# Optimization experiments

Measured on AMD Instinct MI355X. Metric: run time of the kernel, lower is better.

## Reference

```python
import jax, jax.numpy as jnp
import numpy as np

T, B, E, H, V = 128, 64, 300, 2048, 50000


def setup_inputs() -> dict:
    key = jax.random.key(0)
    ks = jax.random.split(key, 7)
    tokens = jax.random.randint(ks[0], (T, B), 0, V, dtype=jnp.int32)
    lens = jax.random.randint(ks[1], (B,), 1, T + 1, dtype=jnp.int32)  # lens >= 1 (assert 0 not in lens)
    embed_table = jax.random.normal(ks[2], (V, E), dtype=jnp.float32) * 0.1
    W_ih = jax.random.normal(ks[3], (4 * H, E), dtype=jnp.float32) * 0.02
    W_hh = jax.random.normal(ks[4], (4 * H, H), dtype=jnp.float32) * 0.02
    b_ih = jax.random.normal(ks[5], (4 * H,), dtype=jnp.float32) * 0.02
    b_hh = jax.random.normal(ks[6], (4 * H,), dtype=jnp.float32) * 0.02
    return {"tokens": tokens, "lens": lens, "embed_table": embed_table,
            "W_ih": W_ih, "W_hh": W_hh, "b_ih": b_ih, "b_hh": b_hh}


def _lstm_scan(xs, W_ih, W_hh, bias, reverse):
    # xs: [T, B, E]; returns all hidden states [T, B, H] (in scan order) and final (h, c)
    hdim = W_hh.shape[1]
    bsz = xs.shape[1]
    h0 = jnp.zeros((bsz, hdim), xs.dtype)
    c0 = jnp.zeros((bsz, hdim), xs.dtype)

    def step(carry, x):
        h, c = carry
        gates = x @ W_ih.T + h @ W_hh.T + bias  # [B, 4H]
        i, f, g, o = jnp.split(gates, 4, axis=-1)  # PyTorch LSTMCell gate order: i, f, g, o
        i = jax.nn.sigmoid(i)
        f = jax.nn.sigmoid(f)
        g = jnp.tanh(g)
        o = jax.nn.sigmoid(o)
        c = f * c + i * g
        h = o * jnp.tanh(c)
        return (h, c), h

    (h_fin, c_fin), hs = jax.lax.scan(step, (h0, c0), xs, reverse=reverse)
    return hs, h_fin


def reference(tokens, lens, embed_table, W_ih, W_hh, b_ih, b_hh):
    # tokens: [T, B] int ids (time-major, matching input_[i] loop over dim 0)
    x = embed_table[tokens]  # [T, B, E]
    bias = b_ih + b_hh
    hs_fwd, _ = _lstm_scan(x, W_ih, W_hh, bias, reverse=False)   # [T, B, H]
    _, h_bwd = _lstm_scan(x, W_ih, W_hh, bias, reverse=True)     # [B, H], same shared cell
    bsz = tokens.shape[1]
    # forward hidden at the last valid timestep of each example (lens - 1)
    last_fwd = hs_fwd[lens - 1, jnp.arange(bsz)]  # [B, H]
    return jnp.concatenate([last_fwd, h_bwd], axis=1)  # [B, 2H]
```

## Files before the change

kernel.cpp:

```cpp
#include <hip/hip_runtime.h>
#include <math.h>

#define T_ 128
#define B_ 64
#define E_ 300
#define H_ 2048

#define K1   2368
#define XKS  10
#define NKS  74
#define APELEMS 19398656ull
#define BXELEMS 5242880ull
#define BHPING  524288ull

typedef __attribute__((ext_vector_type(8))) short short8;
typedef __attribute__((ext_vector_type(4))) float float4v;

__device__ __forceinline__ unsigned f2bf(float f) {
    unsigned u = __float_as_uint(f);
    return (u + 0x7FFFu + ((u >> 16) & 1u)) >> 16;
}
__device__ __forceinline__ float bf2f(unsigned b) { return __uint_as_float(b << 16); }

__device__ __forceinline__ void gl_lds16(const void* g, void* l) {
    __builtin_amdgcn_global_load_lds(
        (const __attribute__((address_space(1))) unsigned int*)g,
        (__attribute__((address_space(3))) unsigned int*)l, 16, 0, 0);
}

__device__ __forceinline__ float sigm(float x) { return 1.f / (1.f + expf(-x)); }


__global__ void init2(short* __restrict__ Bh, float* __restrict__ cb) {
    const int nB = 2 * (int)BHPING;
    const int nC = 2 * 2048 * 64;
    int stride = gridDim.x * blockDim.x;
    int i = blockIdx.x * blockDim.x + threadIdx.x;
    for (int idx = i; idx < nB; idx += stride) Bh[idx] = 0;
    for (int idx = i; idx < nC; idx += stride) cb[idx] = 0.f;
}

__global__ void pack_w(const float* __restrict__ Wih, const float* __restrict__ Whh,
                       short* __restrict__ Ahi, short* __restrict__ Alo) {
    long long idx = (long long)blockIdx.x * blockDim.x + threadIdx.x;
    if (idx >= (long long)APELEMS) return;
    int j  = (int)(idx & 7);
    int l  = (int)((idx >> 3) & 63);
    int mf = (int)((idx >> 9) & 7);
    int rest = (int)(idx >> 12);
    int ks = rest % 74;
    int rb = rest / 74;
    int row = rb * 128 + mf * 16 + (l & 15);
    int kr  = ks * 32 + (l >> 4) * 8 + j;
    float wv = 0.f;
    if (kr < 300)       wv = Wih[(size_t)row * 300 + kr];
    else if (kr >= 320) wv = Whh[(size_t)row * 2048 + (kr - 320)];
    unsigned hb = f2bf(wv);
    Ahi[idx] = (short)hb;
    Alo[idx] = (short)f2bf(wv - bf2f(hb));
}

__global__ void pack_x(const int* __restrict__ tokens, const float* __restrict__ embed,
                       short* __restrict__ Bx) {
    long long idx = (long long)blockIdx.x * blockDim.x + threadIdx.x;
    if (idx >= (long long)BXELEMS) return;
    int j   = (int)(idx & 7);
    int l   = (int)((idx >> 3) & 63);
    int nf4 = (int)((idx >> 9) & 3);
    int hl  = (int)((idx >> 11) & 1);
    int rest = (int)(idx >> 12);
    int ks = rest % 10;
    int tt = rest / 10;
    int b  = nf4 * 16 + (l & 15);
    int kr = ks * 32 + (l >> 4) * 8 + j;
    float v = 0.f;
    if (kr < 300) {
        int tok = tokens[tt * 64 + b];
        v = embed[(size_t)tok * 300 + kr];
    }
    unsigned hb = f2bf(v);
    Bx[idx] = hl ? (short)f2bf(v - bf2f(hb)) : (short)hb;
}

template<int BLD>
__device__ __forceinline__ void stage_tile(
    const short* __restrict__ Ap, const short* __restrict__ Bx,
    const short* __restrict__ Bh, short* lds,
    int mb, int ks, int buf, int t, int ping, int tid)
{
    short* As = lds + buf * 12288;
    short* Bs = As + 4096;
#pragma unroll
    for (int q = 0; q < 2; ++q) {
        int lid = q * 256 + tid;
        gl_lds16(Ap + (size_t)(mb * 74 + ks) * 4096 + lid * 8, As + lid * 8);
    }
#pragma unroll
    for (int q = 0; q < BLD; ++q) {
        int lid = q * 256 + tid;
        int g = lid >> 6, ll = lid & 63;
        int dsel, hl, nf4;
        if (BLD == 2) { dsel = g >> 2; hl = 0;            nf4 = g & 3; }
        else          { dsel = g >> 3; hl = (g >> 2) & 1; nf4 = g & 3; }
        const short* src;
        if (ks < XKS) {
            int xt = dsel ? (127 - t) : t;
            src = Bx + (((size_t)(xt * 10 + ks) * 2 + hl) * 4 + nf4) * 512 + ll * 8;
        } else {
            src = Bh + (size_t)ping * BHPING
                + ((size_t)(ks - 10) * 16 + (dsel * 2 + hl) * 4 + nf4) * 512 + ll * 8;
        }
        gl_lds16(src, Bs + lid * 8);
    }
}

__global__ __launch_bounds__(256, 2) void gemm_step(
    const short* __restrict__ Ahi, const short* __restrict__ Alo,
    const short* __restrict__ Bx, const short* __restrict__ Bh,
    float* __restrict__ p, int t)
{
    __shared__ short lds[36864];
    const int bb = (int)blockIdx.x;
    const int mb = bb >> 3, s = bb & 7;
    const int tid = (int)threadIdx.x;
    const int w = tid >> 6, l = tid & 63;
    const int wm = w >> 1, wn = w & 1;
    const int ping = t & 1;
    const int ks0 = (s < 2) ? s * 10 : 20 + (s - 2) * 9;
    const int nks = (s < 2) ? 10 : 9;

    float4v acc[4][4];
#pragma unroll
    for (int i = 0; i < 4; ++i)
#pragma unroll
        for (int n = 0; n < 4; ++n) acc[i][n] = (float4v){0.f, 0.f, 0.f, 0.f};

    stage_tile<4>(Ahi, Bx, Bh, lds, mb, ks0,     0, t, ping, tid);
    stage_tile<4>(Ahi, Bx, Bh, lds, mb, ks0 + 1, 1, t, ping, tid);
    asm volatile("s_waitcnt vmcnt(6)" ::: "memory");
    __builtin_amdgcn_s_barrier();
    __builtin_amdgcn_sched_barrier(0);

    for (int it = 0; it < nks; ++it) {
        const int buf = it % 3;
        stage_tile<4>(Ahi, Bx, Bh, lds, mb, ks0 + it + 2, (it + 2) % 3, t, ping, tid);

        short* As = lds + buf * 12288;
        short* Bs = As + 4096;
        short8 a[4], bf[8];
#pragma unroll
        for (int i = 0; i < 4; ++i)
            a[i] = *(const short8*)(As + ((wm * 4 + i) * 64 + l) * 8);
#pragma unroll
        for (int j = 0; j < 8; ++j)
            bf[j] = *(const short8*)(Bs + ((wn * 8 + j) * 64 + l) * 8);
        __builtin_amdgcn_s_setprio(1);
#pragma unroll
        for (int i = 0; i < 4; ++i)
#pragma unroll
            for (int hl = 0; hl < 2; ++hl)
#pragma unroll
                for (int n = 0; n < 4; ++n)
                    acc[i][n] = __builtin_amdgcn_mfma_f32_16x16x32_bf16(
                        a[i], bf[hl * 4 + n], acc[i][n], 0, 0, 0);
        __builtin_amdgcn_s_setprio(0);

        asm volatile("s_waitcnt vmcnt(6)" ::: "memory");
        __builtin_amdgcn_s_barrier();
        __builtin_amdgcn_sched_barrier(0);
    }
    asm volatile("s_waitcnt vmcnt(0)" ::: "memory");
    __builtin_amdgcn_s_barrier();
    __builtin_amdgcn_sched_barrier(0);

    stage_tile<2>(Alo, Bx, Bh, lds, mb, ks0,     0, t, ping, tid);
    stage_tile<2>(Alo, Bx, Bh, lds, mb, ks0 + 1, 1, t, ping, tid);
    asm volatile("s_waitcnt vmcnt(4)" ::: "memory");
    __builtin_amdgcn_s_barrier();
    __builtin_amdgcn_sched_barrier(0);

    for (int it = 0; it < nks; ++it) {
        const int buf = it % 3;
        stage_tile<2>(Alo, Bx, Bh, lds, mb, ks0 + it + 2, (it + 2) % 3, t, ping, tid);

        short* As = lds + buf * 12288;
        short* Bs = As + 4096;
        short8 a[4], bf[4];
#pragma unroll
        for (int i = 0; i < 4; ++i)
            a[i] = *(const short8*)(As + ((wm * 4 + i) * 64 + l) * 8);
#pragma unroll
        for (int n = 0; n < 4; ++n)
            bf[n] = *(const short8*)(Bs + ((wn * 4 + n) * 64 + l) * 8);
        __builtin_amdgcn_s_setprio(1);
#pragma unroll
        for (int i = 0; i < 4; ++i)
#pragma unroll
            for (int n = 0; n < 4; ++n)
                acc[i][n] = __builtin_amdgcn_mfma_f32_16x16x32_bf16(
                    a[i], bf[n], acc[i][n], 0, 0, 0);
        __builtin_amdgcn_s_setprio(0);

        asm volatile("s_waitcnt vmcnt(4)" ::: "memory");
        __builtin_amdgcn_s_barrier();
        __builtin_amdgcn_sched_barrier(0);
    }
    asm volatile("s_waitcnt vmcnt(0)" ::: "memory");
    __builtin_amdgcn_s_barrier();
    __builtin_amdgcn_sched_barrier(0);

#pragma unroll
    for (int i = 0; i < 4; ++i)
#pragma unroll
        for (int n = 0; n < 4; ++n)
#pragma unroll
            for (int r = 0; r < 4; ++r) {
                int row = mb * 128 + wm * 64 + i * 16 + (l >> 4) * 4 + r;
                int col = wn * 64 + n * 16 + (l & 15);
                p[((size_t)s * 8192 + row) * 128 + col] = acc[i][n][r];
            }
}

__global__ __launch_bounds__(256) void update2(
    const float* __restrict__ p,
    const float* __restrict__ b_ih, const float* __restrict__ b_hh,
    const int* __restrict__ lens,
    float* __restrict__ cbuf,
    short* __restrict__ Bh,
    float* __restrict__ out, int t)
{
    int tid0 = blockIdx.x * 256 + threadIdx.x;
    for (int item = tid0; item < 262144; item += 65536) {
        int b = item & 63, k = (item >> 6) & 2047, dir = item >> 17;
        float g[4];
#pragma unroll
        for (int gg = 0; gg < 4; ++gg) {
            int row = gg * 2048 + k;
            float v = 0.f;
#pragma unroll
            for (int s = 0; s < 8; ++s) v += p[((size_t)s * 8192 + row) * 128 + dir * 64 + b];
            g[gg] = v + b_ih[row] + b_hh[row];
        }
        float iv = sigm(g[0]);
        float fv = sigm(g[1]);
        float gv = tanhf(g[2]);
        float ov = sigm(g[3]);
        size_t cidx = ((size_t)dir * 2048 + k) * 64 + b;
        float c = fv * cbuf[cidx] + iv * gv;
        cbuf[cidx] = c;
        float h = ov * tanhf(c);

        int kk = k & 31, ksh = k >> 5;
        int jj = kk & 7, ll = (kk >> 3) * 16 + (b & 15), sub = b >> 4;
        int pingW = (t + 1) & 1;
        size_t baseh = (size_t)pingW * BHPING + ((size_t)ksh * 16 + (dir * 2) * 4 + sub) * 512 + ll * 8 + jj;
        size_t basel = (size_t)pingW * BHPING + ((size_t)ksh * 16 + (dir * 2 + 1) * 4 + sub) * 512 + ll * 8 + jj;
        unsigned hb = f2bf(h);
        Bh[baseh] = (short)hb;
        Bh[basel] = (short)f2bf(h - bf2f(hb));

        if (dir == 0) { if (t == lens[b] - 1) out[(size_t)b * 4096 + k] = h; }
        else          { if (t == 127)         out[(size_t)b * 4096 + 2048 + k] = h; }
    }
}

#define R2K1    2368
#define R2EPAD  304
#define R2HOFF  304
#define R2HEND  2352
#define R2SEGSTEPS 74
#define R2REALSTEPS 222
#define R2SPLITSTEPS 56

__global__ void init_ws2(short* __restrict__ hb, float* __restrict__ cb,
                         short* __restrict__ zer) {
    const int nH = 2 * 2 * 2 * 64 * 2048;
    const int nC = 2 * 2048 * 64;
    int stride = gridDim.x * blockDim.x;
    int i = blockIdx.x * blockDim.x + threadIdx.x;
    for (int idx = i; idx < nH; idx += stride) hb[idx] = 0;
    for (int idx = i; idx < nC; idx += stride) cb[idx] = 0.f;
    for (int idx = i; idx < 128; idx += stride) zer[idx] = 0;
}

__global__ void conv_w(const float* __restrict__ Wih, const float* __restrict__ Whh,
                       short* __restrict__ whi, short* __restrict__ wlo) {
    int idx = blockIdx.x * blockDim.x + threadIdx.x;
    const int total = 8192 * R2K1;
    if (idx >= total) return;
    int j = idx / R2K1;
    int col = idx - j * R2K1;
    float w = 0.f;
    if (col < E_) w = Wih[(size_t)j * E_ + col];
    else if (col >= R2HOFF && col < R2HEND) w = Whh[(size_t)j * H_ + (col - R2HOFF)];
    unsigned hb = f2bf(w);
    whi[idx] = (short)hb;
    wlo[idx] = (short)f2bf(w - bf2f(hb));
}

__global__ void conv_x(const int* __restrict__ tokens, const float* __restrict__ embed,
                       short* __restrict__ xhi, short* __restrict__ xlo) {
    int idx = blockIdx.x * blockDim.x + threadIdx.x;
    const int total = T_ * B_ * R2EPAD;
    if (idx >= total) return;
    int t = idx / (B_ * R2EPAD);
    int r = idx - t * (B_ * R2EPAD);
    int bb = r / R2EPAD;
    int e = r - bb * R2EPAD;
    float v = 0.f;
    if (e < E_) {
        int tok = tokens[t * B_ + bb];
        v = embed[(size_t)tok * E_ + e];
    }
    unsigned hb = f2bf(v);
    xhi[idx] = (short)hb;
    xlo[idx] = (short)f2bf(v - bf2f(hb));
}

__global__ __launch_bounds__(512) void gemm_partial(
    const short* __restrict__ Whi, const short* __restrict__ Wlo,
    const short* __restrict__ xhi, const short* __restrict__ xlo,
    const short* __restrict__ hbuf,
    const short* __restrict__ zeros,
    float* __restrict__ pbuf, int t)
{
    __shared__ short As[2][8192];
    __shared__ short Bs[2][2048];

    const int bx  = blockIdx.x;
    const int s   = bx & 3;
    const int kt  = (bx >> 2) & 31;
    const int dir = bx >> 7;
    const int tid = threadIdx.x;
    const int w   = tid >> 6;
    const int l   = tid & 63;
    const int ping = t & 1;
    const int xt   = dir ? (T_ - 1 - t) : t;

    int jA[2], cA[2];
#pragma unroll
    for (int q = 0; q < 2; ++q) {
        int idx = (w * 2 + q) * 64 + l;
        cA[q] = idx >> 8;
        int row = idx & 255;
        jA[q] = (row >> 6) * 2048 + kt * 64 + (row & 63);
    }
    int cB = 0, bB = 0;
    if (w < 4) { int idx = w * 64 + l; cB = idx >> 6; bB = idx & 63; }

    const int lhi = l >> 4, llo = l & 15;
    const int rowbase = (w >> 1) * 64 + (w & 1) * 32;

    float4v acc[2][4];
#pragma unroll
    for (int a = 0; a < 2; ++a)
#pragma unroll
        for (int b = 0; b < 4; ++b) acc[a][b] = (float4v){0.f, 0.f, 0.f, 0.f};

    auto stage = [&](int g, int buf) {
        const bool dummy = (g >= R2REALSTEPS);
        const int seg = dummy ? 2 : g / R2SEGSTEPS;
        const int ss  = dummy ? 0 : g - seg * R2SEGSTEPS;
        const int kbase = ss * 32;
        const short* Wsel = (seg < 2) ? Whi : Wlo;
        const int hl = (seg == 1) ? 1 : 0;
        const short* xsel = (seg == 1) ? xlo : xhi;
        const short* hsel = hbuf + (((size_t)ping * 2 + hl) * 2 + dir) * (64 * 2048);
#pragma unroll
        for (int q = 0; q < 2; ++q) {
            const short* src = Wsel + (size_t)jA[q] * R2K1 + kbase + 8 * cA[q];
            gl_lds16(src, &As[buf][(w * 2 + q) * 64 * 8]);
        }
        if (w < 4) {
            int row8 = kbase + 8 * cB;
            const short* src;
            if (dummy || row8 >= R2HEND) src = zeros;
            else if (row8 < R2EPAD)      src = xsel + ((size_t)xt * 64 + bB) * R2EPAD + row8;
            else                         src = hsel + (size_t)bB * 2048 + (row8 - R2HOFF);
            gl_lds16(src, &Bs[buf][w * 64 * 8]);
        }
    };

    const int g0 = s * R2SPLITSTEPS;
    stage(g0, 0);

    for (int it = 0; it < R2SPLITSTEPS; ++it) {
        const int buf = it & 1;
        if (it + 1 < R2SPLITSTEPS) stage(g0 + it + 1, buf ^ 1);
        __syncthreads();
        short8 a0 = *(const short8*)&As[buf][(lhi * 256 + rowbase + llo) * 8];
        short8 a1 = *(const short8*)&As[buf][(lhi * 256 + rowbase + 16 + llo) * 8];
        short8 b0 = *(const short8*)&Bs[buf][(lhi * 64 + llo) * 8];
        short8 b1 = *(const short8*)&Bs[buf][(lhi * 64 + 16 + llo) * 8];
        short8 b2 = *(const short8*)&Bs[buf][(lhi * 64 + 32 + llo) * 8];
        short8 b3 = *(const short8*)&Bs[buf][(lhi * 64 + 48 + llo) * 8];
        acc[0][0] = __builtin_amdgcn_mfma_f32_16x16x32_bf16(a0, b0, acc[0][0], 0, 0, 0);
        acc[0][1] = __builtin_amdgcn_mfma_f32_16x16x32_bf16(a0, b1, acc[0][1], 0, 0, 0);
        acc[0][2] = __builtin_amdgcn_mfma_f32_16x16x32_bf16(a0, b2, acc[0][2], 0, 0, 0);
        acc[0][3] = __builtin_amdgcn_mfma_f32_16x16x32_bf16(a0, b3, acc[0][3], 0, 0, 0);
        acc[1][0] = __builtin_amdgcn_mfma_f32_16x16x32_bf16(a1, b0, acc[1][0], 0, 0, 0);
        acc[1][1] = __builtin_amdgcn_mfma_f32_16x16x32_bf16(a1, b1, acc[1][1], 0, 0, 0);
        acc[1][2] = __builtin_amdgcn_mfma_f32_16x16x32_bf16(a1, b2, acc[1][2], 0, 0, 0);
        acc[1][3] = __builtin_amdgcn_mfma_f32_16x16x32_bf16(a1, b3, acc[1][3], 0, 0, 0);
        __syncthreads();
    }

    float* pb = pbuf + (((size_t)(dir * 32 + kt) * 4 + s) * 256) * 64;
#pragma unroll
    for (int qm = 0; qm < 2; ++qm)
#pragma unroll
        for (int nb = 0; nb < 4; ++nb)
#pragma unroll
            for (int r = 0; r < 4; ++r) {
                int row = rowbase + qm * 16 + lhi * 4 + r;
                int col = nb * 16 + llo;
                pb[row * 64 + col] = acc[qm][nb][r];
            }
}

__global__ __launch_bounds__(256) void lstm_update(
    const float* __restrict__ pbuf,
    const float* __restrict__ b_ih, const float* __restrict__ b_hh,
    const int* __restrict__ lens,
    float* __restrict__ cbuf,
    short* __restrict__ hbuf,
    float* __restrict__ out, int t)
{
    const int bx = blockIdx.x;
    const int kt = bx & 31, dir = bx >> 5;
    const float* pb = pbuf + (size_t)(dir * 32 + kt) * 4 * 256 * 64;
    const int ping = (t + 1) & 1;

    for (int idx = threadIdx.x; idx < 4096; idx += 256) {
        const int q = idx >> 6, bb = idx & 63;
        const int k = kt * 64 + q;
        float gv[4];
#pragma unroll
        for (int gg = 0; gg < 4; ++gg) {
            const int r = gg * 64 + q;
            float v = 0.f;
#pragma unroll
            for (int s2 = 0; s2 < 4; ++s2) v += pb[(s2 * 256 + r) * 64 + bb];
            const int j = gg * 2048 + k;
            gv[gg] = v + b_ih[j] + b_hh[j];
        }
        const float iv = sigm(gv[0]);
        const float fv = sigm(gv[1]);
        const float g2 = tanhf(gv[2]);
        const float ov = sigm(gv[3]);
        const size_t cidx = ((size_t)dir * 2048 + k) * 64 + bb;
        const float c = fv * cbuf[cidx] + iv * g2;
        cbuf[cidx] = c;
        const float h = ov * tanhf(c);

        const unsigned hb = f2bf(h);
        const float hhi = bf2f(hb);
        const unsigned lb = f2bf(h - hhi);
        const size_t basehi = (((size_t)ping * 2 + 0) * 2 + dir) * (64 * 2048);
        const size_t baselo = (((size_t)ping * 2 + 1) * 2 + dir) * (64 * 2048);
        hbuf[basehi + (size_t)bb * 2048 + k] = (short)hb;
        hbuf[baselo + (size_t)bb * 2048 + k] = (short)lb;

        if (dir == 0) {
            if (t == lens[bb] - 1) out[(size_t)bb * (2 * H_) + k] = h;
        } else {
            if (t == T_ - 1) out[(size_t)bb * (2 * H_) + H_ + k] = h;
        }
    }
}

__global__ void init_state(float* __restrict__ hbuf, float* __restrict__ cbuf) {
    int n_h = 2 * 2 * H_ * B_;
    int n_c = 2 * H_ * B_;
    int stride = gridDim.x * blockDim.x;
    int i = blockIdx.x * blockDim.x + threadIdx.x;
    for (int idx = i; idx < n_h; idx += stride) hbuf[idx] = 0.f;
    for (int idx = i; idx < n_c; idx += stride) cbuf[idx] = 0.f;
}

__global__ void gather_x(const int* __restrict__ tokens, const float* __restrict__ embed,
                         float* __restrict__ x_t) {
    int idx = blockIdx.x * blockDim.x + threadIdx.x;
    int total = T_ * E_ * B_;
    if (idx >= total) return;
    int b = idx % B_;
    int r = idx / B_;
    int e = r % E_;
    int t = r / E_;
    int tok = tokens[t * B_ + b];
    x_t[idx] = embed[tok * E_ + e];
}

__global__ __launch_bounds__(256) void lstm_step(
    const float* __restrict__ x_t, const float* __restrict__ W_ih,
    const float* __restrict__ W_hh, const float* __restrict__ b_ih,
    const float* __restrict__ b_hh, const int* __restrict__ lens,
    const float* __restrict__ h_in, float* __restrict__ h_out,
    float* __restrict__ cbuf, float* __restrict__ out, int t)
{
    const int dir = blockIdx.x >> 8;
    const int kblk = blockIdx.x & 255;
    const int bpair = threadIdx.x & 31;
    const int kloc = threadIdx.x >> 5;
    const int k = kblk * 8 + kloc;
    const int b0 = bpair * 2;
    const int xt = dir ? (T_ - 1 - t) : t;
    const float* xrow = x_t + (size_t)xt * E_ * B_;
    const float* hrow = h_in + (size_t)dir * H_ * B_;
    float a0x = 0.f, a0y = 0.f, a1x = 0.f, a1y = 0.f;
    float a2x = 0.f, a2y = 0.f, a3x = 0.f, a3y = 0.f;
    {
        const float* w0 = W_ih + (size_t)(0 * H_ + k) * E_;
        const float* w1 = W_ih + (size_t)(1 * H_ + k) * E_;
        const float* w2 = W_ih + (size_t)(2 * H_ + k) * E_;
        const float* w3 = W_ih + (size_t)(3 * H_ + k) * E_;
#pragma unroll 4
        for (int kk = 0; kk < E_; ++kk) {
            float2 xv = *(const float2*)(xrow + kk * B_ + b0);
            float c0 = w0[kk], c1 = w1[kk], c2 = w2[kk], c3 = w3[kk];
            a0x += xv.x * c0; a0y += xv.y * c0;
            a1x += xv.x * c1; a1y += xv.y * c1;
            a2x += xv.x * c2; a2y += xv.y * c2;
            a3x += xv.x * c3; a3y += xv.y * c3;
        }
    }
    {
        const float* w0 = W_hh + (size_t)(0 * H_ + k) * H_;
        const float* w1 = W_hh + (size_t)(1 * H_ + k) * H_;
        const float* w2 = W_hh + (size_t)(2 * H_ + k) * H_;
        const float* w3 = W_hh + (size_t)(3 * H_ + k) * H_;
#pragma unroll 4
        for (int kk = 0; kk < H_; ++kk) {
            float2 hv = *(const float2*)(hrow + kk * B_ + b0);
            float c0 = w0[kk], c1 = w1[kk], c2 = w2[kk], c3 = w3[kk];
            a0x += hv.x * c0; a0y += hv.y * c0;
            a1x += hv.x * c1; a1y += hv.y * c1;
            a2x += hv.x * c2; a2y += hv.y * c2;
            a3x += hv.x * c3; a3y += hv.y * c3;
        }
    }
    const int j0 = 0 * H_ + k, j1 = 1 * H_ + k, j2 = 2 * H_ + k, j3 = 3 * H_ + k;
    const float bi = b_ih[j0] + b_hh[j0];
    const float bf = b_ih[j1] + b_hh[j1];
    const float bg = b_ih[j2] + b_hh[j2];
    const float bo = b_ih[j3] + b_hh[j3];
    float* cdir = cbuf + (size_t)dir * H_ * B_;
    float* hdir = h_out + (size_t)dir * H_ * B_;
#pragma unroll
    for (int s = 0; s < 2; ++s) {
        const int b = b0 + s;
        const float ai = (s == 0) ? a0x : a0y;
        const float af = (s == 0) ? a1x : a1y;
        const float ag = (s == 0) ? a2x : a2y;
        const float ao = (s == 0) ? a3x : a3y;
        const float iv = sigm(ai + bi);
        const float fv = sigm(af + bf);
        const float gv = tanhf(ag + bg);
        const float ov = sigm(ao + bo);
        const int sidx = k * B_ + b;
        const float c_old = cdir[sidx];
        const float c_new = fv * c_old + iv * gv;
        cdir[sidx] = c_new;
        const float h_new = ov * tanhf(c_new);
        hdir[sidx] = h_new;
        if (dir == 0) {
            if (t == lens[b] - 1) out[(size_t)b * (2 * H_) + k] = h_new;
        } else {
            if (t == T_ - 1) out[(size_t)b * (2 * H_) + H_ + k] = h_new;
        }
    }
}

extern "C" void kernel_launch(void* const* d_in, const int* in_sizes, int n_in,
                              void* d_out, int out_size, void* d_ws, size_t ws_size,
                              hipStream_t stream) {
    const int*   tokens = (const int*)d_in[0];
    const int*   lens   = (const int*)d_in[1];
    const float* embed  = (const float*)d_in[2];
    const float* W_ih   = (const float*)d_in[3];
    const float* W_hh   = (const float*)d_in[4];
    const float* b_ih   = (const float*)d_in[5];
    const float* b_hh   = (const float*)d_in[6];
    float* out = (float*)d_out;

    short* Ahi = (short*)d_ws;
    short* Alo = Ahi + APELEMS;
    short* BxP = Alo + APELEMS;
    short* BhP = BxP + BXELEMS;
    float* cb2n = (float*)(BhP + 2 * BHPING);
    float* pP   = cb2n + 262144;
    const size_t req_new = (size_t)((char*)(pP + 8388608) - (char*)d_ws);

    const size_t SZ_W  = (size_t)8192 * R2K1;
    const size_t SZ_X  = (size_t)T_ * B_ * R2EPAD;
    const size_t SZ_HB = (size_t)2 * 2 * 2 * 64 * 2048;
    const size_t SZ_CB = (size_t)2 * 2048 * 64;
    const size_t SZ_PB = (size_t)64 * 4 * 256 * 64;
    short* Whi2  = (short*)d_ws;
    short* Wlo2  = Whi2 + SZ_W;
    short* xhiB = Wlo2 + SZ_W;
    short* xloB = xhiB + SZ_X;
    short* hb2  = xloB + SZ_X;
    short* zer  = hb2 + SZ_HB;
    float* cb2  = (float*)(zer + 128);
    float* pbuf = cb2 + SZ_CB;
    const size_t req_r2 = (size_t)((char*)(pbuf + SZ_PB) - (char*)d_ws);

    if (ws_size >= req_new) {
        init2<<<512, 256, 0, stream>>>(BhP, cb2n);
        pack_w<<<(int)((APELEMS + 255) / 256), 256, 0, stream>>>(W_ih, W_hh, Ahi, Alo);
        pack_x<<<(int)((BXELEMS + 255) / 256), 256, 0, stream>>>(tokens, embed, BxP);
        for (int t = 0; t < T_; ++t) {
            gemm_step<<<512, 256, 0, stream>>>(Ahi, Alo, BxP, BhP, pP, t);
            update2<<<256, 256, 0, stream>>>(pP, b_ih, b_hh, lens, cb2n, BhP, out, t);
        }
    } else if (ws_size >= req_r2) {
        init_ws2<<<1024, 256, 0, stream>>>(hb2, cb2, zer);
        {
            int total = 8192 * R2K1;
            conv_w<<<(total + 255) / 256, 256, 0, stream>>>(W_ih, W_hh, Whi2, Wlo2);
        }
        {
            int total = T_ * B_ * R2EPAD;
            conv_x<<<(total + 255) / 256, 256, 0, stream>>>(tokens, embed, xhiB, xloB);
        }
        for (int t = 0; t < T_; ++t) {
            gemm_partial<<<256, 512, 0, stream>>>(Whi2, Wlo2, xhiB, xloB, hb2, zer, pbuf, t);
            lstm_update<<<64, 256, 0, stream>>>(pbuf, b_ih, b_hh, lens, cb2, hb2, out, t);
        }
    } else {
        float* ws   = (float*)d_ws;
        float* x_t  = ws;
        float* hbuf = x_t + (size_t)T_ * E_ * B_;
        float* cbuf = hbuf + (size_t)2 * 2 * H_ * B_;
        init_state<<<256, 256, 0, stream>>>(hbuf, cbuf);
        {
            int total = T_ * E_ * B_;
            gather_x<<<(total + 255) / 256, 256, 0, stream>>>(tokens, embed, x_t);
        }
        for (int t = 0; t < T_; ++t) {
            const float* h_in  = hbuf + (size_t)(t & 1) * 2 * H_ * B_;
            float*       h_out = hbuf + (size_t)((t + 1) & 1) * 2 * H_ * B_;
            lstm_step<<<512, 256, 0, stream>>>(x_t, W_ih, W_hh, b_ih, b_hh, lens,
                                               h_in, h_out, cbuf, out, t);
        }
    }
}
```

Before: 4.017 ms.

## Double M-tile per block with 512 threads, 4-stage LDS ring and register prefetch

The per-step GEMM kernel now uses 512-thread blocks that each cover two 128-row M tiles, which halves the grid and lets each staged B tile be reused by twice as many waves. The LDS pipeline goes from a 3-buffer to a 4-buffer ring with deeper prefetch, and the next tile's fragments are read from LDS into registers before the current MFMAs run. The aim is fewer redundant B loads from global memory and better hiding of global and LDS latency. In exchange it uses about 128KB of LDS per block and more registers, which may lower occupancy.

```diff
diff --git a/kernel.cpp b/kernel.cpp
--- a/kernel.cpp
+++ b/kernel.cpp
@@ -82,46 +82,121 @@
     Bx[idx] = hl ? (short)f2bf(v - bf2f(hb)) : (short)hb;
 }
 
-template<int BLD>
-__device__ __forceinline__ void stage_tile(
+template<int HI>
+__device__ __forceinline__ void run_pass(
     const short* __restrict__ Ap, const short* __restrict__ Bx,
-    const short* __restrict__ Bh, short* lds,
-    int mb, int ks, int buf, int t, int ping, int tid)
+    const short* __restrict__ Bh, short* lds, float4v (&acc)[4][4],
+    int mb2, int ks0, int nks, int t, int ping, int tid, int wm, int wn, int l)
 {
-    short* As = lds + buf * 12288;
-    short* Bs = As + 4096;
-#pragma unroll
-    for (int q = 0; q < 2; ++q) {
-        int lid = q * 256 + tid;
-        gl_lds16(Ap + (size_t)(mb * 74 + ks) * 4096 + lid * 8, As + lid * 8);
-    }
-#pragma unroll
-    for (int q = 0; q < BLD; ++q) {
-        int lid = q * 256 + tid;
-        int g = lid >> 6, ll = lid & 63;
-        int dsel, hl, nf4;
-        if (BLD == 2) { dsel = g >> 2; hl = 0;            nf4 = g & 3; }
-        else          { dsel = g >> 3; hl = (g >> 2) & 1; nf4 = g & 3; }
-        const short* src;
-        if (ks < XKS) {
-            int xt = dsel ? (127 - t) : t;
-            src = Bx + (((size_t)(xt * 10 + ks) * 2 + hl) * 4 + nf4) * 512 + ll * 8;
+    constexpr int BUFSH = 16384;
+    constexpr int NB = HI ? 8 : 4;
+
+    auto stage = [&](int ks, int buf) {
+        short* As = lds + buf * BUFSH;
+        short* Bs = As + 8192;
+#pragma unroll
+        for (int q = 0; q < 2; ++q) {
+            int lid = q * 512 + tid;
+            int rbo = lid >> 9;
+            gl_lds16(Ap + ((size_t)((mb2 * 2 + rbo) * 74 + ks) * 512 + (lid & 511)) * 8,
+                     As + lid * 8);
+        }
+#pragma unroll
+        for (int q = 0; q < (HI ? 2 : 1); ++q) {
+            int lid = q * 512 + tid;
+            int g = lid >> 6, ll = lid & 63;
+            int dsel, hl, nf4;
+            if (HI) { dsel = g >> 3; hl = (g >> 2) & 1; nf4 = g & 3; }
+            else    { dsel = g >> 2; hl = 0;            nf4 = g & 3; }
+            const short* src;
+            if (ks < XKS) {
+                int xt = dsel ? (127 - t) : t;
+                src = Bx + (((size_t)(xt * 10 + ks) * 2 + hl) * 4 + nf4) * 512 + ll * 8;
+            } else {
+                src = Bh + (size_t)ping * BHPING
+                    + ((size_t)(ks - 10) * 16 + (dsel * 2 + hl) * 4 + nf4) * 512 + ll * 8;
+            }
+            gl_lds16(src, Bs + lid * 8);
+        }
+    };
+
+    stage(ks0, 0);
+    stage(ks0 + 1, 1);
+    stage(ks0 + 2, 2);
+    if constexpr (HI) { asm volatile("s_waitcnt vmcnt(4)" ::: "memory"); }
+    else              { asm volatile("s_waitcnt vmcnt(3)" ::: "memory"); }
+    __builtin_amdgcn_s_barrier();
+    __builtin_amdgcn_sched_barrier(0);
+
+    short8 ac[4], bc[NB];
+    {
+        short* As = lds;
+        short* Bs = lds + 8192;
+#pragma unroll
+        for (int i = 0; i < 4; ++i)
+            ac[i] = *(const short8*)(As + ((wm * 4 + i) * 64 + l) * 8);
+#pragma unroll
+        for (int n = 0; n < NB; ++n)
+            bc[n] = *(const short8*)(Bs + ((wn * NB + n) * 64 + l) * 8);
+    }
+
+    for (int it = 0; it < nks; ++it) {
+        stage(ks0 + it + 3, (it + 3) & 3);
+
+        short8 an[4], bn[NB];
+        {
+            short* As = lds + ((it + 1) & 3) * BUFSH;
+            short* Bs = As + 8192;
+#pragma unroll
+            for (int i = 0; i < 4; ++i)
+                an[i] = *(const short8*)(As + ((wm * 4 + i) * 64 + l) * 8);
+#pragma unroll
+            for (int n = 0; n < NB; ++n)
+                bn[n] = *(const short8*)(Bs + ((wn * NB + n) * 64 + l) * 8);
+        }
+
+        __builtin_amdgcn_s_setprio(1);
+        if constexpr (HI) {
+#pragma unroll
+            for (int i = 0; i < 4; ++i)
+#pragma unroll
+                for (int j = 0; j < 8; ++j)
+                    acc[i][j & 3] = __builtin_amdgcn_mfma_f32_16x16x32_bf16(
+                        ac[i], bc[j], acc[i][j & 3], 0, 0, 0);
         } else {
-            src = Bh + (size_t)ping * BHPING
-                + ((size_t)(ks - 10) * 16 + (dsel * 2 + hl) * 4 + nf4) * 512 + ll * 8;
-        }
-        gl_lds16(src, Bs + lid * 8);
-    }
-}
-
-__global__ __launch_bounds__(256, 2) void gemm_step(
+#pragma unroll
+            for (int i = 0; i < 4; ++i)
+#pragma unroll
+                for (int n = 0; n < 4; ++n)
+                    acc[i][n] = __builtin_amdgcn_mfma_f32_16x16x32_bf16(
+                        ac[i], bc[n], acc[i][n], 0, 0, 0);
+        }
+        __builtin_amdgcn_s_setprio(0);
+
+#pragma unroll
+        for (int i = 0; i < 4; ++i) ac[i] = an[i];
+#pragma unroll
+        for (int n = 0; n < NB; ++n) bc[n] = bn[n];
+
+        if constexpr (HI) { asm volatile("s_waitcnt vmcnt(4)" ::: "memory"); }
+        else              { asm volatile("s_waitcnt vmcnt(3)" ::: "memory"); }
+        __builtin_amdgcn_s_barrier();
+        __builtin_amdgcn_sched_barrier(0);
+    }
+
+    asm volatile("s_waitcnt vmcnt(0) lgkmcnt(0)" ::: "memory");
+    __builtin_amdgcn_s_barrier();
+    __builtin_amdgcn_sched_barrier(0);
+}
+
+__global__ __launch_bounds__(512, 2) void gemm_step(
     const short* __restrict__ Ahi, const short* __restrict__ Alo,
     const short* __restrict__ Bx, const short* __restrict__ Bh,
     float* __restrict__ p, int t)
 {
-    __shared__ short lds[36864];
+    __shared__ short lds[65536];
     const int bb = (int)blockIdx.x;
-    const int mb = bb >> 3, s = bb & 7;
+    const int mb2 = bb >> 3, s = bb & 7;
     const int tid = (int)threadIdx.x;
     const int w = tid >> 6, l = tid & 63;
     const int wm = w >> 1, wn = w & 1;
@@ -135,87 +210,16 @@
 #pragma unroll
         for (int n = 0; n < 4; ++n) acc[i][n] = (float4v){0.f, 0.f, 0.f, 0.f};
 
-    stage_tile<4>(Ahi, Bx, Bh, lds, mb, ks0,     0, t, ping, tid);
-    stage_tile<4>(Ahi, Bx, Bh, lds, mb, ks0 + 1, 1, t, ping, tid);
-    asm volatile("s_waitcnt vmcnt(6)" ::: "memory");
-    __builtin_amdgcn_s_barrier();
-    __builtin_amdgcn_sched_barrier(0);
-
-    for (int it = 0; it < nks; ++it) {
-        const int buf = it % 3;
-        stage_tile<4>(Ahi, Bx, Bh, lds, mb, ks0 + it + 2, (it + 2) % 3, t, ping, tid);
-
-        short* As = lds + buf * 12288;
-        short* Bs = As + 4096;
-        short8 a[4], bf[8];
-#pragma unroll
-        for (int i = 0; i < 4; ++i)
-            a[i] = *(const short8*)(As + ((wm * 4 + i) * 64 + l) * 8);
-#pragma unroll
-        for (int j = 0; j < 8; ++j)
-            bf[j] = *(const short8*)(Bs + ((wn * 8 + j) * 64 + l) * 8);
-        __builtin_amdgcn_s_setprio(1);
-#pragma unroll
-        for (int i = 0; i < 4; ++i)
-#pragma unroll
-            for (int hl = 0; hl < 2; ++hl)
-#pragma unroll
-                for (int n = 0; n < 4; ++n)
-                    acc[i][n] = __builtin_amdgcn_mfma_f32_16x16x32_bf16(
-                        a[i], bf[hl * 4 + n], acc[i][n], 0, 0, 0);
-        __builtin_amdgcn_s_setprio(0);
-
-        asm volatile("s_waitcnt vmcnt(6)" ::: "memory");
-        __builtin_amdgcn_s_barrier();
-        __builtin_amdgcn_sched_barrier(0);
-    }
-    asm volatile("s_waitcnt vmcnt(0)" ::: "memory");
-    __builtin_amdgcn_s_barrier();
-    __builtin_amdgcn_sched_barrier(0);
-
-    stage_tile<2>(Alo, Bx, Bh, lds, mb, ks0,     0, t, ping, tid);
-    stage_tile<2>(Alo, Bx, Bh, lds, mb, ks0 + 1, 1, t, ping, tid);
-    asm volatile("s_waitcnt vmcnt(4)" ::: "memory");
-    __builtin_amdgcn_s_barrier();
-    __builtin_amdgcn_sched_barrier(0);
-
-    for (int it = 0; it < nks; ++it) {
-        const int buf = it % 3;
-        stage_tile<2>(Alo, Bx, Bh, lds, mb, ks0 + it + 2, (it + 2) % 3, t, ping, tid);
-
-        short* As = lds + buf * 12288;
-        short* Bs = As + 4096;
-        short8 a[4], bf[4];
-#pragma unroll
-        for (int i = 0; i < 4; ++i)
-            a[i] = *(const short8*)(As + ((wm * 4 + i) * 64 + l) * 8);
+    run_pass<1>(Ahi, Bx, Bh, lds, acc, mb2, ks0, nks, t, ping, tid, wm, wn, l);
+    run_pass<0>(Alo, Bx, Bh, lds, acc, mb2, ks0, nks, t, ping, tid, wm, wn, l);
+
+#pragma unroll
+    for (int i = 0; i < 4; ++i)
 #pragma unroll
         for (int n = 0; n < 4; ++n)
-            bf[n] = *(const short8*)(Bs + ((wn * 4 + n) * 64 + l) * 8);
-        __builtin_amdgcn_s_setprio(1);
-#pragma unroll
-        for (int i = 0; i < 4; ++i)
-#pragma unroll
-            for (int n = 0; n < 4; ++n)
-                acc[i][n] = __builtin_amdgcn_mfma_f32_16x16x32_bf16(
-                    a[i], bf[n], acc[i][n], 0, 0, 0);
-        __builtin_amdgcn_s_setprio(0);
-
-        asm volatile("s_waitcnt vmcnt(4)" ::: "memory");
-        __builtin_amdgcn_s_barrier();
-        __builtin_amdgcn_sched_barrier(0);
-    }
-    asm volatile("s_waitcnt vmcnt(0)" ::: "memory");
-    __builtin_amdgcn_s_barrier();
-    __builtin_amdgcn_sched_barrier(0);
-
-#pragma unroll
-    for (int i = 0; i < 4; ++i)
-#pragma unroll
-        for (int n = 0; n < 4; ++n)
 #pragma unroll
             for (int r = 0; r < 4; ++r) {
-                int row = mb * 128 + wm * 64 + i * 16 + (l >> 4) * 4 + r;
+                int row = mb2 * 256 + wm * 64 + i * 16 + (l >> 4) * 4 + r;
                 int col = wn * 64 + n * 16 + (l & 15);
                 p[((size_t)s * 8192 + row) * 128 + col] = acc[i][n][r];
             }
@@ -611,7 +615,7 @@
         pack_w<<<(int)((APELEMS + 255) / 256), 256, 0, stream>>>(W_ih, W_hh, Ahi, Alo);
         pack_x<<<(int)((BXELEMS + 255) / 256), 256, 0, stream>>>(tokens, embed, BxP);
         for (int t = 0; t < T_; ++t) {
-            gemm_step<<<512, 256, 0, stream>>>(Ahi, Alo, BxP, BhP, pP, t);
+            gemm_step<<<256, 512, 0, stream>>>(Ahi, Alo, BxP, BhP, pP, t);
             update2<<<256, 256, 0, stream>>>(pP, b_ih, b_hh, lens, cb2n, BhP, out, t);
         }
     } else if (ws_size >= req_r2) {
```

New measurement: 4.305 ms. 7.2% more time.
